# Kernel optimization log

Measured on AMD Instinct MI355X. Metric: run time of the kernel, lower is better.

Reference implementation:

```python
import jax, jax.numpy as jnp
import numpy as np

B, N, E = 8, 5000, 100000
IN_DIM, OUT_DIM = 128, 128
EPS = 1e-5


def setup_inputs() -> dict:
    key = jax.random.key(0)
    ks = jax.random.split(key, 8)
    node_features = jax.random.normal(ks[0], (B, N, IN_DIM), dtype=jnp.float32)
    edge_index = jax.random.randint(ks[1], (B, 2, E), 0, N, dtype=jnp.int32)
    node_mask = jnp.ones((B, N), dtype=jnp.float32)
    edge_mask = jnp.ones((B, E), dtype=jnp.float32)
    s = 1.0 / np.sqrt(IN_DIM)
    W_self = jax.random.uniform(ks[2], (IN_DIM, OUT_DIM), minval=-s, maxval=s, dtype=jnp.float32)
    b_self = jax.random.uniform(ks[3], (OUT_DIM,), minval=-s, maxval=s, dtype=jnp.float32)
    W_nb = jax.random.uniform(ks[4], (IN_DIM, OUT_DIM), minval=-s, maxval=s, dtype=jnp.float32)
    b_nb = jax.random.uniform(ks[5], (OUT_DIM,), minval=-s, maxval=s, dtype=jnp.float32)
    gamma = jnp.ones((OUT_DIM,), dtype=jnp.float32)
    beta = jnp.zeros((OUT_DIM,), dtype=jnp.float32)
    return {"node_features": node_features, "edge_index": edge_index,
            "node_mask": node_mask, "edge_mask": edge_mask,
            "W_self": W_self, "b_self": b_self, "W_nb": W_nb, "b_nb": b_nb,
            "gamma": gamma, "beta": beta}


def _aggregate_mean(x, ei, em):
    # x: [N, D], ei: [2, E], em: [E]. Masked segment-mean over incoming edges.
    src, tgt = ei[0], ei[1]
    sf = x[src] * em[:, None]                                   # [E, D]
    sums = jax.ops.segment_sum(sf, tgt, num_segments=N)         # [N, D]
    cnt = jax.ops.segment_sum(em, tgt, num_segments=N)          # [N]
    return sums / jnp.maximum(cnt, 1.0)[:, None]


def reference(node_features, edge_index, node_mask, edge_mask,
              W_self, b_self, W_nb, b_nb, gamma, beta):
    self_feat = jnp.einsum('bnd,do->bno', node_features, W_self) + b_self
    agg = jax.vmap(_aggregate_mean)(node_features, edge_index, edge_mask)  # [B,N,D]
    nb_feat = jnp.einsum('bnd,do->bno', agg, W_nb) + b_nb
    out = jax.nn.relu(self_feat + nb_feat)
    # dropout in eval mode -> identity
    mu = jnp.mean(out, axis=-1, keepdims=True)
    var = jnp.var(out, axis=-1, keepdims=True)
    out = (out - mu) * jax.lax.rsqrt(var + EPS) * gamma + beta
    return out * node_mask[..., None]
```

## Files before the change

kernel.cpp:

```cpp
#include <hip/hip_runtime.h>


#define B_ 8
#define N_ 5000
#define E_ 100000
#define D_ 128
#define EPS_ 1e-5f
#define NNODES (B_ * N_)
#define NEDGES (B_ * E_)
#define JB 313
#define PPB ((E_ / 2 + 255) / 256)
#define FILL_BLOCKS (8 * PPB)
#define CONV_BLOCKS 2500
#define CAP 64
#define LDSP 136

typedef __bf16 bf16x8 __attribute__((ext_vector_type(8)));
typedef float  f32x4  __attribute__((ext_vector_type(4)));

static __device__ __forceinline__ unsigned short f2bf(float f) {
    union { float f; unsigned int i; } c; c.f = f;
    unsigned int i = c.i;
    i += 0x7fffu + ((i >> 16) & 1u);
    return (unsigned short)(i >> 16);
}
static __device__ __forceinline__ float bflo(unsigned int u) {
    return __uint_as_float(u << 16);
}
static __device__ __forceinline__ float bfhi(unsigned int u) {
    return __uint_as_float(u & 0xffff0000u);
}

__global__ __launch_bounds__(256) void fill_k(
    const int* __restrict__ ei, const float* __restrict__ em,
    int* __restrict__ cnt, unsigned int* __restrict__ entries,
    const float* __restrict__ x, unsigned short* __restrict__ xbf,
    const float* __restrict__ Wself, const float* __restrict__ Wnb,
    unsigned short* __restrict__ Bt)
{
    int blk = blockIdx.x;
    if (blk < FILL_BLOCKS) {
        int b = blk & 7;
        int p = (blk >> 3) * 256 + threadIdx.x;
        if (p >= E_ / 2) return;
        int e = 2 * p;
        const int* eib = ei + (size_t)b * 2 * E_;
        int2   sv = *(const int2*)(eib + e);
        int2   tv = *(const int2*)(eib + E_ + e);
        float2 mv = *(const float2*)(em + (size_t)b * E_ + e);
        int gb = b * N_;
        if (mv.x != 0.0f) {
            int g = gb + tv.x;
            int slot = atomicAdd(&cnt[g], 1);
            if (slot < CAP)
                entries[((size_t)g << 6) + slot] =
                    (unsigned int)(gb + sv.x) | ((unsigned int)f2bf(mv.x) << 16);
        }
        if (mv.y != 0.0f) {
            int g = gb + tv.y;
            int slot = atomicAdd(&cnt[g], 1);
            if (slot < CAP)
                entries[((size_t)g << 6) + slot] =
                    (unsigned int)(gb + sv.y) | ((unsigned int)f2bf(mv.y) << 16);
        }
    } else if (blk < FILL_BLOCKS + CONV_BLOCKS) {
        size_t base = (size_t)(blk - FILL_BLOCKS) * 2048 + threadIdx.x * 8;
        float4 va = *(const float4*)(x + base);
        float4 vb = *(const float4*)(x + base + 4);
        uint4 o;
        o.x = (unsigned int)f2bf(va.x) | ((unsigned int)f2bf(va.y) << 16);
        o.y = (unsigned int)f2bf(va.z) | ((unsigned int)f2bf(va.w) << 16);
        o.z = (unsigned int)f2bf(vb.x) | ((unsigned int)f2bf(vb.y) << 16);
        o.w = (unsigned int)f2bf(vb.z) | ((unsigned int)f2bf(vb.w) << 16);
        *(uint4*)(xbf + base) = o;
    } else {
        int n = blk - FILL_BLOCKS - CONV_BLOCKS;
        int k = threadIdx.x;
        float v = (k < 128) ? Wself[(size_t)k * D_ + n]
                            : Wnb[(size_t)(k - 128) * D_ + n];
        Bt[(size_t)n * 256 + k] = f2bf(v);
    }
}

static __device__ __forceinline__ void gather_node_lds(
    int g, int lane, const unsigned short* __restrict__ xbf,
    const int* __restrict__ cnt, const unsigned int* __restrict__ entries,
    unsigned short* dst)
{
    int dg = cnt[g]; if (dg > CAP) dg = CAP;
    const unsigned int* ep = entries + ((size_t)g << 6);
    int grp = lane >> 4;
    int c8 = lane & 15;

    float a[8];
    #pragma unroll
    for (int i = 0; i < 8; ++i) a[i] = 0.f;
    float cs = 0.f;

    unsigned int ee = (lane < 16 && lane < dg) ? ep[lane] : 0u;
    int k = 0;
    for (; k + 16 <= dg; k += 16) {
        unsigned int een = (lane < 16 && k + 16 + lane < dg) ? ep[k + 16 + lane] : 0u;
        #pragma unroll
        for (int j = 0; j < 4; ++j) {
            unsigned int ej = (unsigned int)__shfl((int)ee, 4 * j + grp, 64);
            int   sj = ej & 0xFFFFu;
            float mj = __uint_as_float(ej & 0xFFFF0000u);
            uint4 v = *(const uint4*)(xbf + (size_t)sj * D_ + 8 * c8);
            a[0] += bflo(v.x) * mj; a[1] += bfhi(v.x) * mj;
            a[2] += bflo(v.y) * mj; a[3] += bfhi(v.y) * mj;
            a[4] += bflo(v.z) * mj; a[5] += bfhi(v.z) * mj;
            a[6] += bflo(v.w) * mj; a[7] += bfhi(v.w) * mj;
            cs += mj;
        }
        ee = een;
    }
    int rem = dg - k;
    if (rem > 0) {
        #pragma unroll
        for (int j = 0; j < 4; ++j) {
            int eidx = 4 * j + grp;
            unsigned int ej = (unsigned int)__shfl((int)ee, eidx, 64);
            int   sj = ej & 0xFFFFu;
            float mj = __uint_as_float(ej & 0xFFFF0000u);
            if (eidx < rem) {
                uint4 v = *(const uint4*)(xbf + (size_t)sj * D_ + 8 * c8);
                a[0] += bflo(v.x) * mj; a[1] += bfhi(v.x) * mj;
                a[2] += bflo(v.y) * mj; a[3] += bfhi(v.y) * mj;
                a[4] += bflo(v.z) * mj; a[5] += bfhi(v.z) * mj;
                a[6] += bflo(v.w) * mj; a[7] += bfhi(v.w) * mj;
                cs += mj;
            }
        }
    }

    #pragma unroll
    for (int q = 0; q < 8; ++q) {
        a[q] += __shfl_xor(a[q], 16, 64);
        a[q] += __shfl_xor(a[q], 32, 64);
    }
    cs += __shfl_xor(cs, 16, 64);
    cs += __shfl_xor(cs, 32, 64);

    if (lane < 16) {
        float inv = 1.0f / fmaxf(cs, 1.0f);
        uint4 o;
        o.x = (unsigned int)f2bf(a[0] * inv) | ((unsigned int)f2bf(a[1] * inv) << 16);
        o.y = (unsigned int)f2bf(a[2] * inv) | ((unsigned int)f2bf(a[3] * inv) << 16);
        o.z = (unsigned int)f2bf(a[4] * inv) | ((unsigned int)f2bf(a[5] * inv) << 16);
        o.w = (unsigned int)f2bf(a[6] * inv) | ((unsigned int)f2bf(a[7] * inv) << 16);
        *(uint4*)(dst + 8 * c8) = o;
    }
}

__global__ __launch_bounds__(256) void fused_k(
    const unsigned short* __restrict__ xbf, const int* __restrict__ cnt,
    const unsigned int* __restrict__ entries,
    const unsigned short* __restrict__ Bt,
    const float* __restrict__ bself, const float* __restrict__ bnb,
    const float* __restrict__ gamma, const float* __restrict__ beta,
    const float* __restrict__ nmask, float* __restrict__ out)
{
    __shared__ unsigned short xs[16][LDSP];
    __shared__ unsigned short as[16][LDSP];
    __shared__ float red[4][2][16];

    int t = threadIdx.x;
    int lane = t & 63, wv = t >> 6;
    int b = blockIdx.x & 7;
    int j = blockIdx.x >> 3;
    int i0 = j * 16;
    int g0 = b * N_ + i0;
    int limit = N_ - i0; if (limit > 16) limit = 16;

    #pragma unroll
    for (int lr = wv * 4; lr < wv * 4 + 4; ++lr) {
        unsigned int v = 0;
        if (lr < limit)
            v = ((const unsigned int*)(xbf + (size_t)(g0 + lr) * D_))[lane];
        ((unsigned int*)&xs[lr][0])[lane] = v;
    }
    for (int lr = wv * 4; lr < wv * 4 + 4; ++lr) {
        if (lr < limit) {
            gather_node_lds(g0 + lr, lane, xbf, cnt, entries, &as[lr][0]);
        } else if (lane < 16) {
            *(uint4*)&as[lr][8 * (lane & 15)] = make_uint4(0u, 0u, 0u, 0u);
        }
    }
    __syncthreads();

    int quad = lane >> 4;
    int lcol = lane & 15;

    f32x4 acc[2];
    acc[0] = (f32x4)0.0f;
    acc[1] = (f32x4)0.0f;

    #pragma unroll
    for (int kk = 0; kk < 4; ++kk) {
        int kof = kk * 32 + quad * 8;
        bf16x8 a = *(const bf16x8*)&xs[lcol][kof];
        #pragma unroll
        for (int p = 0; p < 2; ++p) {
            int tt = wv * 2 + p;
            bf16x8 bf = *(const bf16x8*)(Bt + (size_t)(tt * 16 + lcol) * 256 + kof);
            acc[p] = __builtin_amdgcn_mfma_f32_16x16x32_bf16(a, bf, acc[p], 0, 0, 0);
        }
    }
    #pragma unroll
    for (int kk = 0; kk < 4; ++kk) {
        int kof = kk * 32 + quad * 8;
        bf16x8 a = *(const bf16x8*)&as[lcol][kof];
        #pragma unroll
        for (int p = 0; p < 2; ++p) {
            int tt = wv * 2 + p;
            bf16x8 bf = *(const bf16x8*)(Bt + (size_t)(tt * 16 + lcol) * 256 + 128 + kof);
            acc[p] = __builtin_amdgcn_mfma_f32_16x16x32_bf16(a, bf, acc[p], 0, 0, 0);
        }
    }

    float h[2][4];
    float s[4] = {0, 0, 0, 0}, q[4] = {0, 0, 0, 0};
    float gam[2], bet[2];
    #pragma unroll
    for (int p = 0; p < 2; ++p) {
        int col = (wv * 2 + p) * 16 + lcol;
        float bs = bself[col] + bnb[col];
        gam[p] = gamma[col];
        bet[p] = beta[col];
        #pragma unroll
        for (int r = 0; r < 4; ++r) {
            float v = fmaxf(acc[p][r] + bs, 0.0f);
            h[p][r] = v;
            s[r] += v;
            q[r] += v * v;
        }
    }
    #pragma unroll
    for (int r = 0; r < 4; ++r) {
        #pragma unroll
        for (int off = 1; off <= 8; off <<= 1) {
            s[r] += __shfl_xor(s[r], off, 64);
            q[r] += __shfl_xor(q[r], off, 64);
        }
    }
    if (lcol == 0) {
        #pragma unroll
        for (int r = 0; r < 4; ++r) {
            red[wv][0][quad * 4 + r] = s[r];
            red[wv][1][quad * 4 + r] = q[r];
        }
    }
    __syncthreads();

    #pragma unroll
    for (int r = 0; r < 4; ++r) {
        int row = quad * 4 + r;
        int irow = i0 + row;
        if (irow >= N_) continue;
        float S = red[0][0][row] + red[1][0][row] + red[2][0][row] + red[3][0][row];
        float Q = red[0][1][row] + red[1][1][row] + red[2][1][row] + red[3][1][row];
        float mu = S * (1.0f / D_);
        float var = Q * (1.0f / D_) - mu * mu;
        float rin = rsqrtf(fmaxf(var, 0.0f) + EPS_);
        int g = b * N_ + irow;
        float mk = nmask[g];
        float* op = out + (size_t)g * D_;
        #pragma unroll
        for (int p = 0; p < 2; ++p) {
            int col = (wv * 2 + p) * 16 + lcol;
            op[col] = ((h[p][r] - mu) * rin * gam[p] + bet[p]) * mk;
        }
    }
}

extern "C" void kernel_launch(void* const* d_in, const int* in_sizes, int n_in,
                              void* d_out, int out_size, void* d_ws, size_t ws_size,
                              hipStream_t stream)
{
    const float* x     = (const float*)d_in[0];
    const int*   ei    = (const int*)d_in[1];
    const float* nmask = (const float*)d_in[2];
    const float* em    = (const float*)d_in[3];
    const float* Wself = (const float*)d_in[4];
    const float* bself = (const float*)d_in[5];
    const float* Wnb   = (const float*)d_in[6];
    const float* bnb   = (const float*)d_in[7];
    const float* gamma = (const float*)d_in[8];
    const float* beta  = (const float*)d_in[9];
    float* out = (float*)d_out;

    int* cnt = (int*)d_ws;
    unsigned int* entries = (unsigned int*)(cnt + NNODES);
    unsigned short* Bt = (unsigned short*)(entries + (size_t)NNODES * CAP);
    unsigned short* xbf = Bt + (size_t)128 * 256;

    hipMemsetAsync(cnt, 0, NNODES * sizeof(int), stream);
    fill_k<<<FILL_BLOCKS + CONV_BLOCKS + 128, 256, 0, stream>>>(
        ei, em, cnt, entries, x, xbf, Wself, Wnb, Bt);
    fused_k<<<8 * JB, 256, 0, stream>>>(xbf, cnt, entries, Bt,
                                        bself, bnb, gamma, beta, nmask, out);
}
```

Baseline: 164.6 us.

## Gather four nodes per wave concurrently, one 16-lane group per node

The neighbor-mean gather is restructured so each 16-lane group of a wave handles its own node, instead of the whole wave looping over four nodes serially and splitting edges across groups. Degree and the first edge entries are loaded up front, the edge loop runs in fixed chunks of 16 with predicated zero-weight loads, and it exits early once all groups in the wave are done. This removes the cross-group shuffle reduction and the serialized per-node loop, exposing more independent memory loads in flight. In exchange, groups with fewer edges idle while the highest-degree node in the wave finishes, and masked slots still issue loads of row 0.

```diff
diff --git a/kernel.cpp b/kernel.cpp
--- a/kernel.cpp
+++ b/kernel.cpp
@@ -82,77 +82,6 @@
     }
 }
 
-static __device__ __forceinline__ void gather_node_lds(
-    int g, int lane, const unsigned short* __restrict__ xbf,
-    const int* __restrict__ cnt, const unsigned int* __restrict__ entries,
-    unsigned short* dst)
-{
-    int dg = cnt[g]; if (dg > CAP) dg = CAP;
-    const unsigned int* ep = entries + ((size_t)g << 6);
-    int grp = lane >> 4;
-    int c8 = lane & 15;
-
-    float a[8];
-    #pragma unroll
-    for (int i = 0; i < 8; ++i) a[i] = 0.f;
-    float cs = 0.f;
-
-    unsigned int ee = (lane < 16 && lane < dg) ? ep[lane] : 0u;
-    int k = 0;
-    for (; k + 16 <= dg; k += 16) {
-        unsigned int een = (lane < 16 && k + 16 + lane < dg) ? ep[k + 16 + lane] : 0u;
-        #pragma unroll
-        for (int j = 0; j < 4; ++j) {
-            unsigned int ej = (unsigned int)__shfl((int)ee, 4 * j + grp, 64);
-            int   sj = ej & 0xFFFFu;
-            float mj = __uint_as_float(ej & 0xFFFF0000u);
-            uint4 v = *(const uint4*)(xbf + (size_t)sj * D_ + 8 * c8);
-            a[0] += bflo(v.x) * mj; a[1] += bfhi(v.x) * mj;
-            a[2] += bflo(v.y) * mj; a[3] += bfhi(v.y) * mj;
-            a[4] += bflo(v.z) * mj; a[5] += bfhi(v.z) * mj;
-            a[6] += bflo(v.w) * mj; a[7] += bfhi(v.w) * mj;
-            cs += mj;
-        }
-        ee = een;
-    }
-    int rem = dg - k;
-    if (rem > 0) {
-        #pragma unroll
-        for (int j = 0; j < 4; ++j) {
-            int eidx = 4 * j + grp;
-            unsigned int ej = (unsigned int)__shfl((int)ee, eidx, 64);
-            int   sj = ej & 0xFFFFu;
-            float mj = __uint_as_float(ej & 0xFFFF0000u);
-            if (eidx < rem) {
-                uint4 v = *(const uint4*)(xbf + (size_t)sj * D_ + 8 * c8);
-                a[0] += bflo(v.x) * mj; a[1] += bfhi(v.x) * mj;
-                a[2] += bflo(v.y) * mj; a[3] += bfhi(v.y) * mj;
-                a[4] += bflo(v.z) * mj; a[5] += bfhi(v.z) * mj;
-                a[6] += bflo(v.w) * mj; a[7] += bfhi(v.w) * mj;
-                cs += mj;
-            }
-        }
-    }
-
-    #pragma unroll
-    for (int q = 0; q < 8; ++q) {
-        a[q] += __shfl_xor(a[q], 16, 64);
-        a[q] += __shfl_xor(a[q], 32, 64);
-    }
-    cs += __shfl_xor(cs, 16, 64);
-    cs += __shfl_xor(cs, 32, 64);
-
-    if (lane < 16) {
-        float inv = 1.0f / fmaxf(cs, 1.0f);
-        uint4 o;
-        o.x = (unsigned int)f2bf(a[0] * inv) | ((unsigned int)f2bf(a[1] * inv) << 16);
-        o.y = (unsigned int)f2bf(a[2] * inv) | ((unsigned int)f2bf(a[3] * inv) << 16);
-        o.z = (unsigned int)f2bf(a[4] * inv) | ((unsigned int)f2bf(a[5] * inv) << 16);
-        o.w = (unsigned int)f2bf(a[6] * inv) | ((unsigned int)f2bf(a[7] * inv) << 16);
-        *(uint4*)(dst + 8 * c8) = o;
-    }
-}
-
 __global__ __launch_bounds__(256) void fused_k(
     const unsigned short* __restrict__ xbf, const int* __restrict__ cnt,
     const unsigned int* __restrict__ entries,
@@ -173,6 +102,14 @@
     int g0 = b * N_ + i0;
     int limit = N_ - i0; if (limit > 16) limit = 16;
 
+    int grp = lane >> 4;
+    int c8  = lane & 15;
+    int myrow = (wv << 2) + grp;
+
+    int ga = g0 + ((myrow < limit) ? myrow : 0);
+    int dgr = cnt[ga];
+    unsigned int ee = entries[((size_t)ga << 6) + c8];
+
     #pragma unroll
     for (int lr = wv * 4; lr < wv * 4 + 4; ++lr) {
         unsigned int v = 0;
@@ -180,12 +117,44 @@
             v = ((const unsigned int*)(xbf + (size_t)(g0 + lr) * D_))[lane];
         ((unsigned int*)&xs[lr][0])[lane] = v;
     }
-    for (int lr = wv * 4; lr < wv * 4 + 4; ++lr) {
-        if (lr < limit) {
-            gather_node_lds(g0 + lr, lane, xbf, cnt, entries, &as[lr][0]);
-        } else if (lane < 16) {
-            *(uint4*)&as[lr][8 * (lane & 15)] = make_uint4(0u, 0u, 0u, 0u);
-        }
+
+    int dgg = (myrow < limit) ? ((dgr > CAP) ? CAP : dgr) : 0;
+
+    float a[8];
+    #pragma unroll
+    for (int i = 0; i < 8; ++i) a[i] = 0.f;
+    float cs = 0.f;
+
+    for (int k0 = 0; ; k0 += 16) {
+        unsigned int een = 0u;
+        if (k0 + 16 < CAP)
+            een = entries[((size_t)ga << 6) + (k0 + 16) + c8];
+        #pragma unroll 8
+        for (int k = 0; k < 16; ++k) {
+            unsigned int ej = (unsigned int)__shfl((int)ee, (lane & 48) + k, 64);
+            int   ok = (k0 + k) < dgg;
+            int   sj = ok ? (int)(ej & 0xffffu) : 0;
+            float mj = ok ? __uint_as_float(ej & 0xffff0000u) : 0.0f;
+            uint4 v = *(const uint4*)(xbf + (size_t)sj * D_ + (c8 << 3));
+            a[0] += bflo(v.x) * mj; a[1] += bfhi(v.x) * mj;
+            a[2] += bflo(v.y) * mj; a[3] += bfhi(v.y) * mj;
+            a[4] += bflo(v.z) * mj; a[5] += bfhi(v.z) * mj;
+            a[6] += bflo(v.w) * mj; a[7] += bfhi(v.w) * mj;
+            cs += mj;
+        }
+        if (k0 + 16 >= CAP) break;
+        if (__all(dgg <= k0 + 16)) break;
+        ee = een;
+    }
+
+    {
+        float inv = 1.0f / fmaxf(cs, 1.0f);
+        uint4 o;
+        o.x = (unsigned int)f2bf(a[0] * inv) | ((unsigned int)f2bf(a[1] * inv) << 16);
+        o.y = (unsigned int)f2bf(a[2] * inv) | ((unsigned int)f2bf(a[3] * inv) << 16);
+        o.z = (unsigned int)f2bf(a[4] * inv) | ((unsigned int)f2bf(a[5] * inv) << 16);
+        o.w = (unsigned int)f2bf(a[6] * inv) | ((unsigned int)f2bf(a[7] * inv) << 16);
+        *(uint4*)&as[myrow][c8 << 3] = o;
     }
     __syncthreads();
 
@@ -199,23 +168,23 @@
     #pragma unroll
     for (int kk = 0; kk < 4; ++kk) {
         int kof = kk * 32 + quad * 8;
-        bf16x8 a = *(const bf16x8*)&xs[lcol][kof];
+        bf16x8 av = *(const bf16x8*)&xs[lcol][kof];
         #pragma unroll
         for (int p = 0; p < 2; ++p) {
             int tt = wv * 2 + p;
             bf16x8 bf = *(const bf16x8*)(Bt + (size_t)(tt * 16 + lcol) * 256 + kof);
-            acc[p] = __builtin_amdgcn_mfma_f32_16x16x32_bf16(a, bf, acc[p], 0, 0, 0);
+            acc[p] = __builtin_amdgcn_mfma_f32_16x16x32_bf16(av, bf, acc[p], 0, 0, 0);
         }
     }
     #pragma unroll
     for (int kk = 0; kk < 4; ++kk) {
         int kof = kk * 32 + quad * 8;
-        bf16x8 a = *(const bf16x8*)&as[lcol][kof];
+        bf16x8 av = *(const bf16x8*)&as[lcol][kof];
         #pragma unroll
         for (int p = 0; p < 2; ++p) {
             int tt = wv * 2 + p;
             bf16x8 bf = *(const bf16x8*)(Bt + (size_t)(tt * 16 + lcol) * 256 + 128 + kof);
-            acc[p] = __builtin_amdgcn_mfma_f32_16x16x32_bf16(a, bf, acc[p], 0, 0, 0);
+            acc[p] = __builtin_amdgcn_mfma_f32_16x16x32_bf16(av, bf, acc[p], 0, 0, 0);
         }
     }
 
```

Result: faster. 161.2 us (-2.1%).
